# Optimization experiments

Measured on AMD Instinct MI355X. Metric: run time of the kernel, lower is better.

Reference implementation:

```python
import jax, jax.numpy as jnp
import numpy as np

N_NODES = 100000
N_EDGES = 3200000
NFEAT = 256
HDIM = 64
NCLASS = 64
K = 4
ALPHA = 0.1


def setup_inputs() -> dict:
    key = jax.random.key(0)
    k1, k2, k3, k4, k5, k6 = jax.random.split(key, 6)
    x = jax.random.normal(k1, (N_NODES, NFEAT), dtype=jnp.float32)
    edge_index = jax.random.randint(k2, (2, N_EDGES), 0, N_NODES, dtype=jnp.int64)
    W_in = jax.random.normal(k3, (HDIM, NFEAT), dtype=jnp.float32) * (1.0 / np.sqrt(NFEAT))
    b_in = jax.random.normal(k4, (HDIM,), dtype=jnp.float32) * 0.01
    W_out = jax.random.normal(k5, (NCLASS, HDIM), dtype=jnp.float32) * (1.0 / np.sqrt(HDIM))
    b_out = jax.random.normal(k6, (NCLASS,), dtype=jnp.float32) * 0.01
    return {"x": x, "edge_index": edge_index, "W_in": W_in, "b_in": b_in,
            "W_out": W_out, "b_out": b_out}


def _gcn_norm(edge_index, n_nodes):
    # add self-loops, then symmetric normalization (PyG gcn_norm defaults)
    loops = jnp.arange(n_nodes, dtype=edge_index.dtype)
    src = jnp.concatenate([edge_index[0], loops])
    dst = jnp.concatenate([edge_index[1], loops])
    deg = jax.ops.segment_sum(jnp.ones_like(dst, dtype=jnp.float32), dst,
                              num_segments=n_nodes)
    dinv = jnp.where(deg > 0, 1.0 / jnp.sqrt(deg), 0.0)
    w = dinv[src] * dinv[dst]  # [E+N]
    return src, dst, w


def reference(x, edge_index, W_in, b_in, W_out, b_out):
    n = x.shape[0]
    src, dst, w = _gcn_norm(edge_index, n)
    h = x @ W_in.T + b_in                      # [N, 64]
    x0 = h
    for _ in range(K):                         # APPNP: (1-a) * A_hat h + a * x0
        agg = jax.ops.segment_sum(w[:, None] * h[src], dst, num_segments=n)
        h = (1.0 - ALPHA) * agg + ALPHA * x0
    h = jax.nn.relu(h)
    return h @ W_out.T + b_out                 # [N, nclass]
```

## Files before the change

kernel.cpp:

```cpp
#include <hip/hip_runtime.h>
#include <hip/hip_fp16.h>

#define NN 100000
#define NE 3200000
#define NFEAT 256
#define HDIM 64
#define NCLASS 64
#define ALPHA 0.1f
#define CAP 80

#define NB 256
#define BKN 391
#define EBLK (NE / 256)
#define BCAP 24
#define RCAP 96

typedef _Float16 half8 __attribute__((ext_vector_type(8)));
typedef float f32x4 __attribute__((ext_vector_type(4)));


__global__ __launch_bounds__(1024) void bucket_edges(const int* __restrict__ ei,
                                                     unsigned* __restrict__ pairs,
                                                     int* __restrict__ cntg) {
    __shared__ unsigned buf[NB][BCAP];
    __shared__ int cnt[NB];
    __shared__ int rcur[NB];
    int blk = blockIdx.x;
    int t = threadIdx.x;
    int e0 = blk * EBLK;
    for (int i = t; i < NB; i += 1024) { cnt[i] = 0; rcur[i] = 0; }
    __syncthreads();

    for (int eb = 0; eb < EBLK; eb += 1024) {
        bool act = (eb + t) < EBLK;
        if (act) {
            int e = e0 + eb + t;
            unsigned d = (unsigned)ei[NE + e];
            unsigned src = (unsigned)ei[e];
            unsigned b = d / BKN;
            unsigned w = (src << 9) | (d - b * BKN);
            int p = atomicAdd(&cnt[b], 1);
            if (p < BCAP) buf[b][p] = w;
        }
        __syncthreads();
        int lane = t & 63, wv = t >> 6;
        for (int j = 0; j < 16; j++) {
            int b2 = wv * 16 + j;
            int c = cnt[b2]; if (c > BCAP) c = BCAP;
            int rb = rcur[b2];
            if (lane < c) {
                int idx = rb + lane;
                if (idx < RCAP)
                    pairs[((size_t)blk * NB + b2) * RCAP + idx] = buf[b2][lane];
            }
            if (lane == 0) rcur[b2] = rb + c;
        }
        __syncthreads();
        if (t < NB) cnt[t] = 0;
        __syncthreads();
    }
    if (t < NB) cntg[blk * NB + t] = min(rcur[t], RCAP);
}


__global__ __launch_bounds__(1024) void fill_bucket(const unsigned* __restrict__ pairs,
                                                    const int* __restrict__ cntg,
                                                    int* __restrict__ col,
                                                    int* __restrict__ deg,
                                                    float* __restrict__ dinv) {
    __shared__ int cur[BKN];
    __shared__ int pref[NB + 1];
    __shared__ int cnts[NB];
    int b = blockIdx.x;
    int t = threadIdx.x;
    unsigned lo = (unsigned)b * BKN;
    for (int i = t; i < BKN; i += 1024) cur[i] = 0;
    if (t < NB) cnts[t] = cntg[t * NB + b];
    __syncthreads();
    if (t == 0) {
        int run = 0;
        for (int k = 0; k < NB; k++) { pref[k] = run; run += cnts[k]; }
        pref[NB] = run;
    }
    __syncthreads();
    int T = pref[NB];
    for (int i0 = 0; i0 < T; i0 += 1024) {
        int i = i0 + t;
        if (i < T) {
            int l = 0, h = NB;
            while (h - l > 1) { int m = (l + h) >> 1; if (pref[m] <= i) l = m; else h = m; }
            unsigned w = pairs[((size_t)l * NB + b) * RCAP + (i - pref[l])];
            unsigned dl = w & 511;
            unsigned src = w >> 9;
            int slot = atomicAdd(&cur[dl], 1);
            if (slot < CAP && lo + dl < NN)
                col[(size_t)(lo + dl) * CAP + slot] = (int)src;
        }
    }
    __syncthreads();
    for (int i = t; i < BKN; i += 1024) {
        unsigned node = lo + i;
        if (node < NN) {
            int dgv = cur[i];
            deg[node] = dgv;
            dinv[node] = rsqrtf((float)dgv + 1.f);
        }
    }
}


__global__ void prep_w(const float* __restrict__ W, _Float16* __restrict__ W2g,
                       int KG, int Kfull) {
    int i = blockIdx.x * 256 + threadIdx.x;
    if (i >= KG * 64) return;
    int kg = i >> 6;
    int n = i & 63;
    int slot = (kg << 6) + (n ^ ((kg & 3) << 2));
    _Float16 tmp[8];
#pragma unroll
    for (int j = 0; j < 8; j++) tmp[j] = (_Float16)W[n * Kfull + kg * 8 + j];
    *(half8*)&W2g[(size_t)slot * 8] = *(half8*)tmp;
}


__global__ __launch_bounds__(256) void gemm1_mfma(const float* __restrict__ x,
                                                  const _Float16* __restrict__ W2g,
                                                  const float* __restrict__ bias,
                                                  const float* __restrict__ dinv,
                                                  _Float16* __restrict__ g0) {
    __shared__ _Float16 W2[32 * 64 * 8];
    int t = threadIdx.x;
    for (int i = t; i < 2048; i += 256)
        *(half8*)&W2[(size_t)i * 8] = *(const half8*)&W2g[(size_t)i * 8];
    __syncthreads();

    int lane = t & 63;
    int w = t >> 6;
    int r16 = lane & 15, kg = lane >> 4;
    int row0 = blockIdx.x * 128;
    int rowA = row0 + w * 32 + r16;
    int rowB = rowA + 16;
    int rA = rowA < NN ? rowA : NN - 1;
    int rB = rowB < NN ? rowB : NN - 1;
    const float* pa = &x[(size_t)rA * 256 + kg * 8];
    const float* pb = &x[(size_t)rB * 256 + kg * 8];

    f32x4 acc[2][4];
#pragma unroll
    for (int mt = 0; mt < 2; mt++)
#pragma unroll
        for (int nt = 0; nt < 4; nt++) acc[mt][nt] = (f32x4){0.f, 0.f, 0.f, 0.f};

#pragma unroll
    for (int ks = 0; ks < 8; ks++) {
        float4 va0 = *(const float4*)(pa + ks * 32);
        float4 va1 = *(const float4*)(pa + ks * 32 + 4);
        float4 vb0 = *(const float4*)(pb + ks * 32);
        float4 vb1 = *(const float4*)(pb + ks * 32 + 4);
        _Float16 a0h[8] = {(_Float16)va0.x, (_Float16)va0.y, (_Float16)va0.z, (_Float16)va0.w,
                           (_Float16)va1.x, (_Float16)va1.y, (_Float16)va1.z, (_Float16)va1.w};
        _Float16 a1h[8] = {(_Float16)vb0.x, (_Float16)vb0.y, (_Float16)vb0.z, (_Float16)vb0.w,
                           (_Float16)vb1.x, (_Float16)vb1.y, (_Float16)vb1.z, (_Float16)vb1.w};
        half8 a0 = *(half8*)a0h;
        half8 a1 = *(half8*)a1h;
        int kgg = ks * 4 + kg;
#pragma unroll
        for (int nt = 0; nt < 4; nt++) {
            int nidx = nt * 16 + r16;
            int slot = (kgg << 6) + (nidx ^ ((kgg & 3) << 2));
            half8 bfr = *(half8*)&W2[(size_t)slot * 8];
            acc[0][nt] = __builtin_amdgcn_mfma_f32_16x16x32_f16(a0, bfr, acc[0][nt], 0, 0, 0);
            acc[1][nt] = __builtin_amdgcn_mfma_f32_16x16x32_f16(a1, bfr, acc[1][nt], 0, 0, 0);
        }
    }

#pragma unroll
    for (int mt = 0; mt < 2; mt++)
#pragma unroll
        for (int nt = 0; nt < 4; nt++) {
            int colj = nt * 16 + r16;
            float bv = bias[colj];
#pragma unroll
            for (int r = 0; r < 4; r++) {
                int row = row0 + w * 32 + mt * 16 + kg * 4 + r;
                if (row < NN)
                    g0[(size_t)row * 64 + colj] = (_Float16)((acc[mt][nt][r] + bv) * dinv[row]);
            }
        }
}


__global__ __launch_bounds__(256) void gemm2_mfma(const float* __restrict__ h,
                                                  const _Float16* __restrict__ W2o,
                                                  const float* __restrict__ bias,
                                                  float* __restrict__ out) {
    __shared__ _Float16 W2[8 * 64 * 8];
    int t = threadIdx.x;
    for (int i = t; i < 512; i += 256)
        *(half8*)&W2[(size_t)i * 8] = *(const half8*)&W2o[(size_t)i * 8];
    __syncthreads();

    int lane = t & 63;
    int w = t >> 6;
    int r16 = lane & 15, kg = lane >> 4;
    int row0 = blockIdx.x * 128;
    int rowA = row0 + w * 32 + r16;
    int rowB = rowA + 16;
    int rA = rowA < NN ? rowA : NN - 1;
    int rB = rowB < NN ? rowB : NN - 1;
    const float* pa = &h[(size_t)rA * 64 + kg * 8];
    const float* pb = &h[(size_t)rB * 64 + kg * 8];

    f32x4 acc[2][4];
#pragma unroll
    for (int mt = 0; mt < 2; mt++)
#pragma unroll
        for (int nt = 0; nt < 4; nt++) acc[mt][nt] = (f32x4){0.f, 0.f, 0.f, 0.f};

#pragma unroll
    for (int ks = 0; ks < 2; ks++) {
        float4 va0 = *(const float4*)(pa + ks * 32);
        float4 va1 = *(const float4*)(pa + ks * 32 + 4);
        float4 vb0 = *(const float4*)(pb + ks * 32);
        float4 vb1 = *(const float4*)(pb + ks * 32 + 4);
        _Float16 a0h[8] = {(_Float16)fmaxf(va0.x, 0.f), (_Float16)fmaxf(va0.y, 0.f),
                           (_Float16)fmaxf(va0.z, 0.f), (_Float16)fmaxf(va0.w, 0.f),
                           (_Float16)fmaxf(va1.x, 0.f), (_Float16)fmaxf(va1.y, 0.f),
                           (_Float16)fmaxf(va1.z, 0.f), (_Float16)fmaxf(va1.w, 0.f)};
        _Float16 a1h[8] = {(_Float16)fmaxf(vb0.x, 0.f), (_Float16)fmaxf(vb0.y, 0.f),
                           (_Float16)fmaxf(vb0.z, 0.f), (_Float16)fmaxf(vb0.w, 0.f),
                           (_Float16)fmaxf(vb1.x, 0.f), (_Float16)fmaxf(vb1.y, 0.f),
                           (_Float16)fmaxf(vb1.z, 0.f), (_Float16)fmaxf(vb1.w, 0.f)};
        half8 a0 = *(half8*)a0h;
        half8 a1 = *(half8*)a1h;
        int kgg = ks * 4 + kg;
#pragma unroll
        for (int nt = 0; nt < 4; nt++) {
            int nidx = nt * 16 + r16;
            int slot = (kgg << 6) + (nidx ^ ((kgg & 3) << 2));
            half8 bfr = *(half8*)&W2[(size_t)slot * 8];
            acc[0][nt] = __builtin_amdgcn_mfma_f32_16x16x32_f16(a0, bfr, acc[0][nt], 0, 0, 0);
            acc[1][nt] = __builtin_amdgcn_mfma_f32_16x16x32_f16(a1, bfr, acc[1][nt], 0, 0, 0);
        }
    }

#pragma unroll
    for (int mt = 0; mt < 2; mt++)
#pragma unroll
        for (int nt = 0; nt < 4; nt++) {
            int colj = nt * 16 + r16;
            float bv = bias[colj];
#pragma unroll
            for (int r = 0; r < 4; r++) {
                int row = row0 + w * 32 + mt * 16 + kg * 4 + r;
                if (row < NN)
                    out[(size_t)row * 64 + colj] = acc[mt][nt][r] + bv;
            }
        }
}


template <bool FINAL>
__global__ __launch_bounds__(256) void appnp_prop_h2(const __half* __restrict__ gcur,
                                                     void* __restrict__ gnext,
                                                     const __half* __restrict__ g0,
                                                     const float* __restrict__ dinv,
                                                     const int* __restrict__ deg,
                                                     const int* __restrict__ col) {
    int wid = (blockIdx.x * 256 + threadIdx.x) >> 6;
    int lane = threadIdx.x & 63;
    if (wid >= NN) return;
    int eg = lane >> 3;
    int q  = lane & 7;
    const float4* gc4 = (const float4*)gcur;

    const __half2 hz = __floats2half2_rn(0.f, 0.f);
    __half2 acc[4];
#pragma unroll
    for (int j = 0; j < 4; j++) acc[j] = hz;

    int dg = deg[wid]; if (dg > CAP) dg = CAP;
    int e0 = wid * CAP;
    int end = e0 + dg;
    int p = e0;
    for (; p + 8 < end; p += 16) {
        int i0 = p + eg, i1 = p + 8 + eg;
        bool ok1 = i1 < end;
        int s0 = col[i0];
        int s1 = col[ok1 ? i1 : end - 1];
        float4 r0 = gc4[(size_t)s0 * 8 + q];
        float4 r1 = gc4[(size_t)s1 * 8 + q];
        const __half2* v0 = (const __half2*)&r0;
        const __half2* v1 = (const __half2*)&r1;
#pragma unroll
        for (int j = 0; j < 4; j++) {
            acc[j] = __hadd2(acc[j], v0[j]);
            acc[j] = __hadd2(acc[j], ok1 ? v1[j] : hz);
        }
    }
    if (p < end) {
        int i0 = p + eg;
        bool ok0 = i0 < end;
        int s0 = col[ok0 ? i0 : end - 1];
        float4 r0 = gc4[(size_t)s0 * 8 + q];
        const __half2* v0 = (const __half2*)&r0;
#pragma unroll
        for (int j = 0; j < 4; j++)
            acc[j] = __hadd2(acc[j], ok0 ? v0[j] : hz);
    }

#pragma unroll
    for (int st = 8; st < 64; st <<= 1) {
#pragma unroll
        for (int j = 0; j < 4; j++) {
            int o = __shfl(*(int*)&acc[j], lane ^ st);
            acc[j] = __hadd2(acc[j], *(__half2*)&o);
        }
    }

    if (eg == 0) {
        float di = dinv[wid];
        float k = (1.f - ALPHA) * di * di;
        float4 sraw = gc4[(size_t)wid * 8 + q];
        float4 zraw = ((const float4*)g0)[(size_t)wid * 8 + q];
        const __half2* sh = (const __half2*)&sraw;
        const __half2* zh = (const __half2*)&zraw;
        float g[8];
#pragma unroll
        for (int j = 0; j < 4; j++) {
            float2 a  = __half22float2(acc[j]);
            float2 sf = __half22float2(sh[j]);
            float2 zf = __half22float2(zh[j]);
            g[2 * j]     = k * (a.x + sf.x) + ALPHA * zf.x;
            g[2 * j + 1] = k * (a.y + sf.y) + ALPHA * zf.y;
        }
        if (FINAL) {
            float inv = 1.f / di;
            float* ho = (float*)gnext;
            float4 o0 = make_float4(g[0] * inv, g[1] * inv, g[2] * inv, g[3] * inv);
            float4 o1 = make_float4(g[4] * inv, g[5] * inv, g[6] * inv, g[7] * inv);
            *(float4*)&ho[(size_t)wid * 64 + q * 8]     = o0;
            *(float4*)&ho[(size_t)wid * 64 + q * 8 + 4] = o1;
        } else {
            __half2 h2o[4];
#pragma unroll
            for (int j = 0; j < 4; j++) h2o[j] = __floats2half2_rn(g[2 * j], g[2 * j + 1]);
            *(float4*)&((__half*)gnext)[(size_t)wid * 64 + q * 8] = *(float4*)h2o;
        }
    }
}


extern "C" void kernel_launch(void* const* d_in, const int* in_sizes, int n_in,
                              void* d_out, int out_size, void* d_ws, size_t ws_size,
                              hipStream_t stream) {
    const float* x    = (const float*)d_in[0];
    const int*  ei    = (const int*)d_in[1];
    const float* W_in = (const float*)d_in[2];
    const float* b_in = (const float*)d_in[3];
    const float* W_out= (const float*)d_in[4];
    const float* b_out= (const float*)d_in[5];
    float* out = (float*)d_out;

    char* ws = (char*)d_ws;
    size_t off = 0;
    auto alloc = [&](size_t bytes) -> void* {
        void* p = ws + off;
        off = (off + bytes + 255) & ~(size_t)255;
        return p;
    };
    int*      deg  = (int*)    alloc((size_t)NN * 4);
    float*    dinv = (float*)  alloc((size_t)NN * 4);
    int*      cntg = (int*)    alloc((size_t)NB * 256 * 4);
    _Float16* W2g  = (_Float16*)alloc((size_t)32 * 64 * 8 * 2);
    _Float16* W2o  = (_Float16*)alloc((size_t)8 * 64 * 8 * 2);
    int*      col  = (int*)    alloc((size_t)NN * CAP * 4);
    __half*   g0h  = (__half*) alloc((size_t)NN * HDIM * 2);
    __half*   gA   = (__half*) alloc((size_t)NN * HDIM * 2);
    __half*   gB   = (__half*) alloc((size_t)NN * HDIM * 2);
    unsigned* pairs = (unsigned*)g0h;

    bucket_edges<<<256, 1024, 0, stream>>>(ei, pairs, cntg);
    fill_bucket<<<NB, 1024, 0, stream>>>(pairs, cntg, col, deg, dinv);

    prep_w<<<8, 256, 0, stream>>>(W_in, W2g, 32, 256);
    prep_w<<<2, 256, 0, stream>>>(W_out, W2o, 8, 64);

    gemm1_mfma<<<(NN + 127) / 128, 256, 0, stream>>>(x, W2g, b_in, dinv, (_Float16*)g0h);

    const int pgrid = (NN * HDIM) / 256;
    appnp_prop_h2<false><<<pgrid, 256, 0, stream>>>(g0h, gA, g0h, dinv, deg, col);
    appnp_prop_h2<false><<<pgrid, 256, 0, stream>>>(gA, gB, g0h, dinv, deg, col);
    appnp_prop_h2<false><<<pgrid, 256, 0, stream>>>(gB, gA, g0h, dinv, deg, col);
    appnp_prop_h2<true ><<<pgrid, 256, 0, stream>>>(gA, out, g0h, dinv, deg, col);

    gemm2_mfma<<<(NN + 127) / 128, 256, 0, stream>>>(out, W2o, b_out, out);
}
```

Baseline: 340.3 us.

## Store propagated node features in FP8 to halve gather traffic

Propagation iterates now gather neighbor features stored as FP8 (64 bytes per node) instead of FP16, accumulate in fp32, and write FP8 for the intermediate steps. An extra kernel converts the initial projected features to FP8. Each lane handles 16 features, so 16 edges are processed in parallel per wavefront. This targets the random-gather bandwidth of the four propagation passes, at the cost of a large loss of precision from FP8 storage and more shuffle-reduction work.

```diff
diff --git a/kernel.cpp b/kernel.cpp
--- a/kernel.cpp
+++ b/kernel.cpp
@@ -17,6 +17,27 @@
 
 typedef _Float16 half8 __attribute__((ext_vector_type(8)));
 typedef float f32x4 __attribute__((ext_vector_type(4)));
+
+
+__device__ inline unsigned pack4_fp8(float a, float b, float c, float d) {
+    unsigned v = 0;
+    v = __builtin_amdgcn_cvt_pk_fp8_f32(a, b, v, false);
+    v = __builtin_amdgcn_cvt_pk_fp8_f32(c, d, v, true);
+    return v;
+}
+
+__device__ inline void acc16_fp8(uint4 r, float m, float* acc) {
+    const unsigned* w = (const unsigned*)&r;
+#pragma unroll
+    for (int j = 0; j < 4; j++) {
+        auto lo = __builtin_amdgcn_cvt_pk_f32_fp8(w[j], false);
+        auto hi = __builtin_amdgcn_cvt_pk_f32_fp8(w[j], true);
+        acc[4 * j + 0] = fmaf(m, lo[0], acc[4 * j + 0]);
+        acc[4 * j + 1] = fmaf(m, lo[1], acc[4 * j + 1]);
+        acc[4 * j + 2] = fmaf(m, hi[0], acc[4 * j + 2]);
+        acc[4 * j + 3] = fmaf(m, hi[1], acc[4 * j + 3]);
+    }
+}
 
 
 __global__ __launch_bounds__(1024) void bucket_edges(const int* __restrict__ ei,
@@ -187,6 +208,25 @@
                     g0[(size_t)row * 64 + colj] = (_Float16)((acc[mt][nt][r] + bv) * dinv[row]);
             }
         }
+}
+
+
+__global__ __launch_bounds__(256) void cvt_fp16_fp8(const __half* __restrict__ in,
+                                                    unsigned char* __restrict__ out) {
+    int i = blockIdx.x * 256 + threadIdx.x;
+    if (i >= NN * 8) return;
+    float4 raw = ((const float4*)in)[i];
+    const __half2* h2 = (const __half2*)&raw;
+    float f[8];
+#pragma unroll
+    for (int j = 0; j < 4; j++) {
+        float2 v = __half22float2(h2[j]);
+        f[2 * j] = v.x; f[2 * j + 1] = v.y;
+    }
+    uint2 o;
+    o.x = pack4_fp8(f[0], f[1], f[2], f[3]);
+    o.y = pack4_fp8(f[4], f[5], f[6], f[7]);
+    ((uint2*)out)[i] = o;
 }
 
 
@@ -261,91 +301,101 @@
 
 
 template <bool FINAL>
-__global__ __launch_bounds__(256) void appnp_prop_h2(const __half* __restrict__ gcur,
-                                                     void* __restrict__ gnext,
-                                                     const __half* __restrict__ g0,
-                                                     const float* __restrict__ dinv,
-                                                     const int* __restrict__ deg,
-                                                     const int* __restrict__ col) {
+__global__ __launch_bounds__(256) void appnp_prop_8(const unsigned char* __restrict__ gcur8,
+                                                    void* __restrict__ gnext,
+                                                    const __half* __restrict__ g0h,
+                                                    const float* __restrict__ dinv,
+                                                    const int* __restrict__ deg,
+                                                    const int* __restrict__ col) {
     int wid = (blockIdx.x * 256 + threadIdx.x) >> 6;
     int lane = threadIdx.x & 63;
     if (wid >= NN) return;
-    int eg = lane >> 3;
-    int q  = lane & 7;
-    const float4* gc4 = (const float4*)gcur;
-
-    const __half2 hz = __floats2half2_rn(0.f, 0.f);
-    __half2 acc[4];
-#pragma unroll
-    for (int j = 0; j < 4; j++) acc[j] = hz;
+    int eg = lane >> 2;
+    int q  = lane & 3;
+    const uint4* gc = (const uint4*)gcur8;
+
+    float acc[16];
+#pragma unroll
+    for (int j = 0; j < 16; j++) acc[j] = 0.f;
 
     int dg = deg[wid]; if (dg > CAP) dg = CAP;
     int e0 = wid * CAP;
     int end = e0 + dg;
     int p = e0;
-    for (; p + 8 < end; p += 16) {
-        int i0 = p + eg, i1 = p + 8 + eg;
-        bool ok1 = i1 < end;
+    for (; p + 16 < end; p += 32) {
+        int i0 = p + eg, i1 = p + 16 + eg;
+        float m1 = (i1 < end) ? 1.f : 0.f;
         int s0 = col[i0];
-        int s1 = col[ok1 ? i1 : end - 1];
-        float4 r0 = gc4[(size_t)s0 * 8 + q];
-        float4 r1 = gc4[(size_t)s1 * 8 + q];
-        const __half2* v0 = (const __half2*)&r0;
-        const __half2* v1 = (const __half2*)&r1;
-#pragma unroll
-        for (int j = 0; j < 4; j++) {
-            acc[j] = __hadd2(acc[j], v0[j]);
-            acc[j] = __hadd2(acc[j], ok1 ? v1[j] : hz);
-        }
+        int s1 = col[(i1 < end) ? i1 : end - 1];
+        uint4 r0 = gc[(size_t)s0 * 4 + q];
+        uint4 r1 = gc[(size_t)s1 * 4 + q];
+        acc16_fp8(r0, 1.f, acc);
+        acc16_fp8(r1, m1, acc);
     }
     if (p < end) {
         int i0 = p + eg;
-        bool ok0 = i0 < end;
-        int s0 = col[ok0 ? i0 : end - 1];
-        float4 r0 = gc4[(size_t)s0 * 8 + q];
-        const __half2* v0 = (const __half2*)&r0;
-#pragma unroll
-        for (int j = 0; j < 4; j++)
-            acc[j] = __hadd2(acc[j], ok0 ? v0[j] : hz);
-    }
-
-#pragma unroll
-    for (int st = 8; st < 64; st <<= 1) {
-#pragma unroll
-        for (int j = 0; j < 4; j++) {
-            int o = __shfl(*(int*)&acc[j], lane ^ st);
-            acc[j] = __hadd2(acc[j], *(__half2*)&o);
-        }
+        float m0 = (i0 < end) ? 1.f : 0.f;
+        int s0 = col[(i0 < end) ? i0 : end - 1];
+        uint4 r0 = gc[(size_t)s0 * 4 + q];
+        acc16_fp8(r0, m0, acc);
+    }
+
+#pragma unroll
+    for (int st = 4; st < 64; st <<= 1) {
+#pragma unroll
+        for (int j = 0; j < 16; j++) acc[j] += __shfl(acc[j], lane ^ st);
     }
 
     if (eg == 0) {
         float di = dinv[wid];
         float k = (1.f - ALPHA) * di * di;
-        float4 sraw = gc4[(size_t)wid * 8 + q];
-        float4 zraw = ((const float4*)g0)[(size_t)wid * 8 + q];
-        const __half2* sh = (const __half2*)&sraw;
-        const __half2* zh = (const __half2*)&zraw;
-        float g[8];
-#pragma unroll
-        for (int j = 0; j < 4; j++) {
-            float2 a  = __half22float2(acc[j]);
-            float2 sf = __half22float2(sh[j]);
-            float2 zf = __half22float2(zh[j]);
-            g[2 * j]     = k * (a.x + sf.x) + ALPHA * zf.x;
-            g[2 * j + 1] = k * (a.y + sf.y) + ALPHA * zf.y;
-        }
+        uint4 sraw = gc[(size_t)wid * 4 + q];
+        float sf[16];
+        {
+            const unsigned* w4 = (const unsigned*)&sraw;
+#pragma unroll
+            for (int j = 0; j < 4; j++) {
+                auto lo = __builtin_amdgcn_cvt_pk_f32_fp8(w4[j], false);
+                auto hi = __builtin_amdgcn_cvt_pk_f32_fp8(w4[j], true);
+                sf[4 * j] = lo[0]; sf[4 * j + 1] = lo[1];
+                sf[4 * j + 2] = hi[0]; sf[4 * j + 3] = hi[1];
+            }
+        }
+        float zf[16];
+        {
+            float4 z0 = *(const float4*)&g0h[(size_t)wid * 64 + q * 16];
+            float4 z1 = *(const float4*)&g0h[(size_t)wid * 64 + q * 16 + 8];
+            const __half2* h0 = (const __half2*)&z0;
+            const __half2* h1 = (const __half2*)&z1;
+#pragma unroll
+            for (int j = 0; j < 4; j++) {
+                float2 a = __half22float2(h0[j]);
+                float2 b = __half22float2(h1[j]);
+                zf[2 * j] = a.x; zf[2 * j + 1] = a.y;
+                zf[8 + 2 * j] = b.x; zf[8 + 2 * j + 1] = b.y;
+            }
+        }
+        float g[16];
+#pragma unroll
+        for (int j = 0; j < 16; j++)
+            g[j] = k * (acc[j] + sf[j]) + ALPHA * zf[j];
+
         if (FINAL) {
             float inv = 1.f / di;
             float* ho = (float*)gnext;
-            float4 o0 = make_float4(g[0] * inv, g[1] * inv, g[2] * inv, g[3] * inv);
-            float4 o1 = make_float4(g[4] * inv, g[5] * inv, g[6] * inv, g[7] * inv);
-            *(float4*)&ho[(size_t)wid * 64 + q * 8]     = o0;
-            *(float4*)&ho[(size_t)wid * 64 + q * 8 + 4] = o1;
+#pragma unroll
+            for (int c = 0; c < 4; c++) {
+                float4 o = make_float4(g[4 * c] * inv, g[4 * c + 1] * inv,
+                                       g[4 * c + 2] * inv, g[4 * c + 3] * inv);
+                *(float4*)&ho[(size_t)wid * 64 + q * 16 + c * 4] = o;
+            }
         } else {
-            __half2 h2o[4];
-#pragma unroll
-            for (int j = 0; j < 4; j++) h2o[j] = __floats2half2_rn(g[2 * j], g[2 * j + 1]);
-            *(float4*)&((__half*)gnext)[(size_t)wid * 64 + q * 8] = *(float4*)h2o;
+            uint4 o;
+            o.x = pack4_fp8(g[0], g[1], g[2], g[3]);
+            o.y = pack4_fp8(g[4], g[5], g[6], g[7]);
+            o.z = pack4_fp8(g[8], g[9], g[10], g[11]);
+            o.w = pack4_fp8(g[12], g[13], g[14], g[15]);
+            ((uint4*)gnext)[(size_t)wid * 4 + q] = o;
         }
     }
 }
@@ -376,8 +426,9 @@
     _Float16* W2o  = (_Float16*)alloc((size_t)8 * 64 * 8 * 2);
     int*      col  = (int*)    alloc((size_t)NN * CAP * 4);
     __half*   g0h  = (__half*) alloc((size_t)NN * HDIM * 2);
-    __half*   gA   = (__half*) alloc((size_t)NN * HDIM * 2);
-    __half*   gB   = (__half*) alloc((size_t)NN * HDIM * 2);
+    unsigned char* g08 = (unsigned char*)alloc((size_t)NN * HDIM);
+    unsigned char* gA8 = (unsigned char*)alloc((size_t)NN * HDIM);
+    unsigned char* gB8 = (unsigned char*)alloc((size_t)NN * HDIM);
     unsigned* pairs = (unsigned*)g0h;
 
     bucket_edges<<<256, 1024, 0, stream>>>(ei, pairs, cntg);
@@ -387,12 +438,13 @@
     prep_w<<<2, 256, 0, stream>>>(W_out, W2o, 8, 64);
 
     gemm1_mfma<<<(NN + 127) / 128, 256, 0, stream>>>(x, W2g, b_in, dinv, (_Float16*)g0h);
+    cvt_fp16_fp8<<<(NN * 8 + 255) / 256, 256, 0, stream>>>(g0h, g08);
 
     const int pgrid = (NN * HDIM) / 256;
-    appnp_prop_h2<false><<<pgrid, 256, 0, stream>>>(g0h, gA, g0h, dinv, deg, col);
-    appnp_prop_h2<false><<<pgrid, 256, 0, stream>>>(gA, gB, g0h, dinv, deg, col);
-    appnp_prop_h2<false><<<pgrid, 256, 0, stream>>>(gB, gA, g0h, dinv, deg, col);
-    appnp_prop_h2<true ><<<pgrid, 256, 0, stream>>>(gA, out, g0h, dinv, deg, col);
+    appnp_prop_8<false><<<pgrid, 256, 0, stream>>>(g08, gA8, g0h, dinv, deg, col);
+    appnp_prop_8<false><<<pgrid, 256, 0, stream>>>(gA8, gB8, g0h, dinv, deg, col);
+    appnp_prop_8<false><<<pgrid, 256, 0, stream>>>(gB8, gA8, g0h, dinv, deg, col);
+    appnp_prop_8<true ><<<pgrid, 256, 0, stream>>>(gA8, out, g0h, dinv, deg, col);
 
     gemm2_mfma<<<(NN + 127) / 128, 256, 0, stream>>>(out, W2o, b_out, out);
 }
```

New measurement: 384.3 us. +13.0%, slower.

## Store propagated features in FP8 split into two column halves

Applied to the files above, without the earlier changes.

Propagation buffers change from fp16 rows to fp8 (e4m3 via cvt_pk_fp8), split into two 32-column half arrays. Each block handles one half, so the gathered working set per pass is 3.2MB rather than 12.8MB and fits cache better. Accumulation now runs in fp32. A conversion kernel packs the initial features into fp8, and each edge gather moves 4 bytes per lane instead of 16. The cost is a large precision loss from fp8 storage of unnormalized-scaled features, which could break tolerance, plus twice as many walks over the col lists.

```diff
diff --git a/kernel.cpp b/kernel.cpp
--- a/kernel.cpp
+++ b/kernel.cpp
@@ -17,6 +17,21 @@
 
 typedef _Float16 half8 __attribute__((ext_vector_type(8)));
 typedef float f32x4 __attribute__((ext_vector_type(4)));
+
+
+__device__ inline unsigned pack4_fp8(float a, float b, float c, float d) {
+    unsigned v = 0;
+    v = __builtin_amdgcn_cvt_pk_fp8_f32(a, b, v, false);
+    v = __builtin_amdgcn_cvt_pk_fp8_f32(c, d, v, true);
+    return v;
+}
+
+__device__ inline void acc4_fp8(unsigned r, float m, float* acc) {
+    auto lo = __builtin_amdgcn_cvt_pk_f32_fp8(r, false);
+    auto hi = __builtin_amdgcn_cvt_pk_f32_fp8(r, true);
+    acc[0] = fmaf(m, lo[0], acc[0]); acc[1] = fmaf(m, lo[1], acc[1]);
+    acc[2] = fmaf(m, hi[0], acc[2]); acc[3] = fmaf(m, hi[1], acc[3]);
+}
 
 
 __global__ __launch_bounds__(1024) void bucket_edges(const int* __restrict__ ei,
@@ -187,6 +202,24 @@
                     g0[(size_t)row * 64 + colj] = (_Float16)((acc[mt][nt][r] + bv) * dinv[row]);
             }
         }
+}
+
+
+__global__ __launch_bounds__(256) void cvt_split_fp8(const __half* __restrict__ in,
+                                                     unsigned* __restrict__ outa,
+                                                     unsigned* __restrict__ outb) {
+    int i = blockIdx.x * 256 + threadIdx.x;
+    if (i >= NN * 16) return;
+    int node = i >> 4;
+    int s = i & 15;
+    int half = s >> 3;
+    int q = s & 7;
+    float2 zr = *(const float2*)&in[(size_t)node * 64 + half * 32 + q * 4];
+    const __half2* zh = (const __half2*)&zr;
+    float2 v0 = __half22float2(zh[0]);
+    float2 v1 = __half22float2(zh[1]);
+    unsigned o = pack4_fp8(v0.x, v0.y, v1.x, v1.y);
+    (half ? outb : outa)[(size_t)node * 8 + q] = o;
 }
 
 
@@ -261,91 +294,76 @@
 
 
 template <bool FINAL>
-__global__ __launch_bounds__(256) void appnp_prop_h2(const __half* __restrict__ gcur,
-                                                     void* __restrict__ gnext,
-                                                     const __half* __restrict__ g0,
-                                                     const float* __restrict__ dinv,
-                                                     const int* __restrict__ deg,
-                                                     const int* __restrict__ col) {
-    int wid = (blockIdx.x * 256 + threadIdx.x) >> 6;
+__global__ __launch_bounds__(256) void appnp_prop_s(const unsigned* __restrict__ ga,
+                                                    const unsigned* __restrict__ gb,
+                                                    unsigned* __restrict__ na,
+                                                    unsigned* __restrict__ nb,
+                                                    float* __restrict__ hout,
+                                                    const __half* __restrict__ g0h,
+                                                    const float* __restrict__ dinv,
+                                                    const int* __restrict__ deg,
+                                                    const int* __restrict__ col) {
+    int half = blockIdx.x & 1;
+    int wid = (blockIdx.x >> 1) * 4 + (threadIdx.x >> 6);
     int lane = threadIdx.x & 63;
     if (wid >= NN) return;
+    const unsigned* gc = half ? gb : ga;
     int eg = lane >> 3;
     int q  = lane & 7;
-    const float4* gc4 = (const float4*)gcur;
-
-    const __half2 hz = __floats2half2_rn(0.f, 0.f);
-    __half2 acc[4];
-#pragma unroll
-    for (int j = 0; j < 4; j++) acc[j] = hz;
-
+
+    float acc[4] = {0.f, 0.f, 0.f, 0.f};
     int dg = deg[wid]; if (dg > CAP) dg = CAP;
     int e0 = wid * CAP;
     int end = e0 + dg;
-    int p = e0;
-    for (; p + 8 < end; p += 16) {
-        int i0 = p + eg, i1 = p + 8 + eg;
-        bool ok1 = i1 < end;
-        int s0 = col[i0];
-        int s1 = col[ok1 ? i1 : end - 1];
-        float4 r0 = gc4[(size_t)s0 * 8 + q];
-        float4 r1 = gc4[(size_t)s1 * 8 + q];
-        const __half2* v0 = (const __half2*)&r0;
-        const __half2* v1 = (const __half2*)&r1;
-#pragma unroll
-        for (int j = 0; j < 4; j++) {
-            acc[j] = __hadd2(acc[j], v0[j]);
-            acc[j] = __hadd2(acc[j], ok1 ? v1[j] : hz);
-        }
-    }
-    if (p < end) {
-        int i0 = p + eg;
-        bool ok0 = i0 < end;
-        int s0 = col[ok0 ? i0 : end - 1];
-        float4 r0 = gc4[(size_t)s0 * 8 + q];
-        const __half2* v0 = (const __half2*)&r0;
-#pragma unroll
-        for (int j = 0; j < 4; j++)
-            acc[j] = __hadd2(acc[j], ok0 ? v0[j] : hz);
+    for (int p = e0; p < end; p += 32) {
+        int i0 = p + eg, i1 = p + 8 + eg, i2 = p + 16 + eg, i3 = p + 24 + eg;
+        float m0 = (i0 < end) ? 1.f : 0.f;
+        float m1 = (i1 < end) ? 1.f : 0.f;
+        float m2 = (i2 < end) ? 1.f : 0.f;
+        float m3 = (i3 < end) ? 1.f : 0.f;
+        int s0 = col[(i0 < end) ? i0 : end - 1];
+        int s1 = col[(i1 < end) ? i1 : end - 1];
+        int s2 = col[(i2 < end) ? i2 : end - 1];
+        int s3 = col[(i3 < end) ? i3 : end - 1];
+        unsigned r0 = gc[(size_t)s0 * 8 + q];
+        unsigned r1 = gc[(size_t)s1 * 8 + q];
+        unsigned r2 = gc[(size_t)s2 * 8 + q];
+        unsigned r3 = gc[(size_t)s3 * 8 + q];
+        acc4_fp8(r0, m0, acc);
+        acc4_fp8(r1, m1, acc);
+        acc4_fp8(r2, m2, acc);
+        acc4_fp8(r3, m3, acc);
     }
 
 #pragma unroll
     for (int st = 8; st < 64; st <<= 1) {
 #pragma unroll
-        for (int j = 0; j < 4; j++) {
-            int o = __shfl(*(int*)&acc[j], lane ^ st);
-            acc[j] = __hadd2(acc[j], *(__half2*)&o);
-        }
+        for (int j = 0; j < 4; j++) acc[j] += __shfl(acc[j], lane ^ st);
     }
 
     if (eg == 0) {
         float di = dinv[wid];
         float k = (1.f - ALPHA) * di * di;
-        float4 sraw = gc4[(size_t)wid * 8 + q];
-        float4 zraw = ((const float4*)g0)[(size_t)wid * 8 + q];
-        const __half2* sh = (const __half2*)&sraw;
-        const __half2* zh = (const __half2*)&zraw;
-        float g[8];
-#pragma unroll
-        for (int j = 0; j < 4; j++) {
-            float2 a  = __half22float2(acc[j]);
-            float2 sf = __half22float2(sh[j]);
-            float2 zf = __half22float2(zh[j]);
-            g[2 * j]     = k * (a.x + sf.x) + ALPHA * zf.x;
-            g[2 * j + 1] = k * (a.y + sf.y) + ALPHA * zf.y;
-        }
+        unsigned sraw = gc[(size_t)wid * 8 + q];
+        auto slo = __builtin_amdgcn_cvt_pk_f32_fp8(sraw, false);
+        auto shi = __builtin_amdgcn_cvt_pk_f32_fp8(sraw, true);
+        float sf[4] = {slo[0], slo[1], shi[0], shi[1]};
+        float2 zr = *(const float2*)&g0h[(size_t)wid * 64 + half * 32 + q * 4];
+        const __half2* zh = (const __half2*)&zr;
+        float2 z0 = __half22float2(zh[0]);
+        float2 z1 = __half22float2(zh[1]);
+        float zf[4] = {z0.x, z0.y, z1.x, z1.y};
+        float g[4];
+#pragma unroll
+        for (int j = 0; j < 4; j++)
+            g[j] = k * (acc[j] + sf[j]) + ALPHA * zf[j];
+
         if (FINAL) {
             float inv = 1.f / di;
-            float* ho = (float*)gnext;
-            float4 o0 = make_float4(g[0] * inv, g[1] * inv, g[2] * inv, g[3] * inv);
-            float4 o1 = make_float4(g[4] * inv, g[5] * inv, g[6] * inv, g[7] * inv);
-            *(float4*)&ho[(size_t)wid * 64 + q * 8]     = o0;
-            *(float4*)&ho[(size_t)wid * 64 + q * 8 + 4] = o1;
+            float4 o = make_float4(g[0] * inv, g[1] * inv, g[2] * inv, g[3] * inv);
+            *(float4*)&hout[(size_t)wid * 64 + half * 32 + q * 4] = o;
         } else {
-            __half2 h2o[4];
-#pragma unroll
-            for (int j = 0; j < 4; j++) h2o[j] = __floats2half2_rn(g[2 * j], g[2 * j + 1]);
-            *(float4*)&((__half*)gnext)[(size_t)wid * 64 + q * 8] = *(float4*)h2o;
+            (half ? nb : na)[(size_t)wid * 8 + q] = pack4_fp8(g[0], g[1], g[2], g[3]);
         }
     }
 }
@@ -376,8 +394,12 @@
     _Float16* W2o  = (_Float16*)alloc((size_t)8 * 64 * 8 * 2);
     int*      col  = (int*)    alloc((size_t)NN * CAP * 4);
     __half*   g0h  = (__half*) alloc((size_t)NN * HDIM * 2);
-    __half*   gA   = (__half*) alloc((size_t)NN * HDIM * 2);
-    __half*   gB   = (__half*) alloc((size_t)NN * HDIM * 2);
+    unsigned* g0a  = (unsigned*)alloc((size_t)NN * 32);
+    unsigned* g0b  = (unsigned*)alloc((size_t)NN * 32);
+    unsigned* gAa  = (unsigned*)alloc((size_t)NN * 32);
+    unsigned* gAb  = (unsigned*)alloc((size_t)NN * 32);
+    unsigned* gBa  = (unsigned*)alloc((size_t)NN * 32);
+    unsigned* gBb  = (unsigned*)alloc((size_t)NN * 32);
     unsigned* pairs = (unsigned*)g0h;
 
     bucket_edges<<<256, 1024, 0, stream>>>(ei, pairs, cntg);
@@ -387,12 +409,13 @@
     prep_w<<<2, 256, 0, stream>>>(W_out, W2o, 8, 64);
 
     gemm1_mfma<<<(NN + 127) / 128, 256, 0, stream>>>(x, W2g, b_in, dinv, (_Float16*)g0h);
-
-    const int pgrid = (NN * HDIM) / 256;
-    appnp_prop_h2<false><<<pgrid, 256, 0, stream>>>(g0h, gA, g0h, dinv, deg, col);
-    appnp_prop_h2<false><<<pgrid, 256, 0, stream>>>(gA, gB, g0h, dinv, deg, col);
-    appnp_prop_h2<false><<<pgrid, 256, 0, stream>>>(gB, gA, g0h, dinv, deg, col);
-    appnp_prop_h2<true ><<<pgrid, 256, 0, stream>>>(gA, out, g0h, dinv, deg, col);
+    cvt_split_fp8<<<(NN * 16 + 255) / 256, 256, 0, stream>>>(g0h, g0a, g0b);
+
+    const int pgrid = 2 * (NN / 4);
+    appnp_prop_s<false><<<pgrid, 256, 0, stream>>>(g0a, g0b, gAa, gAb, nullptr, g0h, dinv, deg, col);
+    appnp_prop_s<false><<<pgrid, 256, 0, stream>>>(gAa, gAb, gBa, gBb, nullptr, g0h, dinv, deg, col);
+    appnp_prop_s<false><<<pgrid, 256, 0, stream>>>(gBa, gBb, gAa, gAb, nullptr, g0h, dinv, deg, col);
+    appnp_prop_s<true ><<<pgrid, 256, 0, stream>>>(gAa, gAb, nullptr, nullptr, out, g0h, dinv, deg, col);
 
     gemm2_mfma<<<(NN + 127) / 128, 256, 0, stream>>>(out, W2o, b_out, out);
 }
```

After: 376.3 us. 10.6% more time.
